# Kernel optimization log

Hardware: AMD Instinct MI355X
Metric: run time of the kernel (lower is better)

## Reference

```python
import jax, jax.numpy as jnp
import numpy as np

# Per-species MLP dims from CoefficientLayer._create_model (H, C, N, O), aev_dim=384
DIMS = {"h": [384, 160, 128, 96, 1], "c": [384, 144, 112, 96, 1], "n": [384, 128, 112, 96, 1], "o": [384, 128, 112, 96, 1]}


def setup_inputs() -> dict:
    key = jax.random.key(0)
    B, A, D = 256, 256, 384
    ks = jax.random.split(key, 64)
    inp = {}
    inp["species"] = jax.random.randint(ks[0], (B, A), 0, 4)  # species index 0..3
    inp["aev"] = jax.random.normal(ks[1], (B, A, D), dtype=jnp.float32)
    inp["b0"] = jnp.array([0.1, 0.2, 0.3, 0.4], dtype=jnp.float32)  # shifter intercepts
    inp["b1"] = jnp.array([1.0, 1.1, 0.9, 1.2], dtype=jnp.float32)  # shifter slopes
    ki = 2
    for name, dims in DIMS.items():
        for l in range(4):
            fi, fo = dims[l], dims[l + 1]
            inp[f"{name}w{l}"] = jax.random.normal(ks[ki], (fi, fo), dtype=jnp.float32) / np.float32(np.sqrt(fi))
            ki += 1
            inp[f"{name}b{l}"] = jnp.zeros((fo,), dtype=jnp.float32)
    return inp


def _mlp(x, ws, bs):
    # Linear -> CELU(0.1) x3 -> Linear(->1), squeeze last dim
    for i in range(3):
        x = jax.nn.celu(x @ ws[i] + bs[i], alpha=0.1)
    return (x @ ws[3] + bs[3])[..., 0]


def reference(species, aev, b0, b1,
              hw0, hb0, hw1, hb1, hw2, hb2, hw3, hb3,
              cw0, cb0, cw1, cb1, cw2, cb2, cw3, cb3,
              nw0, nb0, nw1, nb1, nw2, nb2, nw3, nb3,
              ow0, ob0, ow1, ob1, ow2, ob2, ow3, ob3):
    nets = [
        ([hw0, hw1, hw2, hw3], [hb0, hb1, hb2, hb3]),
        ([cw0, cw1, cw2, cw3], [cb0, cb1, cb2, cb3]),
        ([nw0, nw1, nw2, nw3], [nb0, nb1, nb2, nb3]),
        ([ow0, ow1, ow2, ow3], [ob0, ob1, ob2, ob3]),
    ]
    # ANIModel hard routing: each atom's coefficient comes from its species' network;
    # atoms with species == -1 (padding) stay 0.
    coef = jnp.zeros(species.shape, dtype=aev.dtype)
    for i, (ws, bs) in enumerate(nets):  # fixed small loop over 4 species
        coef = jnp.where(species == i, _mlp(aev, ws, bs), coef)
    # Shifter: result[mask_i] = b0[i] + b1[i] * coef[mask_i]; padding stays 0
    idx = jnp.clip(species, 0)
    return jnp.where(species >= 0, b0[idx] + b1[idx] * coef, jnp.zeros((), dtype=aev.dtype))
```

## Files before the change

kernel.cpp:

```cpp
#include <hip/hip_runtime.h>

typedef _Float16 f16;
typedef _Float16 f16x8 __attribute__((ext_vector_type(8)));
typedef float f32x4 __attribute__((ext_vector_type(4)));
typedef unsigned short u16;
typedef unsigned int u32;

#define NATOMS 65536
#define CAP 17920

#define WS_LISTS_OFF 256
#define WS_W_OFF 524544
#define WS_W_ELEMS 350208
#define WS_ACT0_OFF (2u << 20)
#define WS_BIG (46u << 20)

#define BLK0 128
#define BLK12 64

#define ROWB 1536
#define TILEB (16 * ROWB)
#define FRAGS 24

struct ConvJob { const float* src; int K, N, KS, NT, CK, off; };

struct PrepParams {
  const int* species;
  int* counts;
  u16* lists;
  f16* wbase;
  ConvJob jobs[16];
};

struct GemmParams {
  const float* aev;
  const float* b0;
  const float* b1;
  const float* bias[4][4];
  const float* w3src[4];
  const f16* w[4][4];
  const int* counts;
  const u16* lists;
  f16* act0;
  float* out;
  int Nreal0[4];
  int Nreal1[4];
};

template <int N> struct AF { f16x8 v[N]; };

__global__ __launch_bounds__(256) void prep_kernel(PrepParams p) {
  int tid = threadIdx.x;
  if (blockIdx.x < 256) {
    __shared__ int wcnt[4][4];
    __shared__ int wbase[4][4];
    int i = blockIdx.x * 256 + tid;
    int s = p.species[i];
    int wave = tid >> 6, lane = tid & 63;
    unsigned long long m[4];
    #pragma unroll
    for (int t = 0; t < 4; t++) {
      m[t] = __ballot(s == t);
      if (lane == 0) wcnt[wave][t] = __popcll(m[t]);
    }
    __syncthreads();
    if (tid < 4) {
      int t = tid;
      int c0 = wcnt[0][t], c1 = wcnt[1][t], c2 = wcnt[2][t], c3 = wcnt[3][t];
      int base = atomicAdd(&p.counts[t], c0 + c1 + c2 + c3);
      wbase[0][t] = base;
      wbase[1][t] = base + c0;
      wbase[2][t] = base + c0 + c1;
      wbase[3][t] = base + c0 + c1 + c2;
    }
    __syncthreads();
    int rnk = __popcll(m[s] & ((1ull << lane) - 1ull));
    p.lists[s * NATOMS + wbase[wave][s] + rnk] = (u16)i;
  } else {
    int bx = blockIdx.x - 256;
    int job = bx / 30, bxin = bx - job * 30;
    ConvJob jb = p.jobs[job];
    int e = bxin * 256 + tid;
    int nslots = jb.KS * jb.NT * 64;
    if (e >= nslots) return;
    int frag = e >> 6, lane = e & 63;
    int c = frag / (jb.CK * jb.NT);
    int rem = frag - c * (jb.CK * jb.NT);
    int ckc = min(jb.CK, jb.KS - c * jb.CK);
    int nt = rem / ckc, ki = rem - nt * ckc;
    int ks = c * jb.CK + ki;
    int q = lane >> 4, nlo = lane & 15;
    int n = nt * 16 + nlo;
    int k0 = ks * 32 + q * 8;
    f16x8 v;
    #pragma unroll
    for (int j = 0; j < 8; j++) {
      int k = k0 + j;
      float x = (n < jb.N && k < jb.K) ? jb.src[k * jb.N + n] : 0.f;
      v[j] = (f16)x;
    }
    *(f16x8*)(p.wbase + jb.off + (size_t)e * 8) = v;
  }
}

__device__ __forceinline__ float celu01(float v) {
  return v > 0.f ? v : 0.1f * (__expf(v * 10.f) - 1.f);
}

__device__ __forceinline__ void stage_frag(const f16* g, f16* l, int lane) {
  __builtin_amdgcn_global_load_lds(
      (const __attribute__((address_space(1))) u32*)(g + lane * 8),
      (__attribute__((address_space(3))) u32*)l, 16, 0, 0);
}

__device__ __forceinline__ void dma16(const void* g, void* l) {
  __builtin_amdgcn_global_load_lds(
      (const __attribute__((address_space(1))) u32*)g,
      (__attribute__((address_space(3))) u32*)l, 16, 0, 0);
}

template <int NT0>
__device__ void k0_body(const GemmParams& p, int s, int bl, char* smem) {
  int tid = threadIdx.x, w = tid >> 6, lane = tid & 63;
  int q = lane >> 4, nlo = lane & 15;
  int cnt = min(p.counts[s], CAP);
  int ntiles = (cnt + 15) >> 4;
  int tpb = (ntiles + BLK0 - 1) / BLK0;
  int t0 = bl * tpb;
  int nt_blk = min(ntiles - t0, tpb);
  if (nt_blk <= 0) return;

  const u16* list = p.lists + s * NATOMS;
  u16* atoms_l = (u16*)(smem + 3 * TILEB);

  f16x8 wf[12];
  float bv = 0.f;
  if (w < NT0) {
    const f16* wg = p.w[s][0];
    #pragma unroll
    for (int ks = 0; ks < 12; ks++)
      wf[ks] = *(const f16x8*)(wg + (size_t)(ks * NT0 + w) * 512 + lane * 8);
    int n = w * 16 + nlo;
    bv = (n < p.Nreal0[s]) ? p.bias[s][0][n] : 0.f;
  }
  f16* act = p.act0 + (size_t)s * CAP * 160;

  for (int idx = tid; idx < nt_blk * 16; idx += 640)
    atoms_l[idx] = list[min(t0 * 16 + idx, cnt - 1)];
  __syncthreads();

  auto stage = [&](int i) {
    char* buf = smem + (i % 3) * TILEB;
    #pragma unroll
    for (int j = 0; j < 3; j++) {
      int f = min(w * 3 + j, FRAGS - 1);
      int o = f * 1024 + lane * 16;
      int row = o / ROWB;
      int intra = o - row * ROWB;
      int gin = intra ^ ((row & 7) << 4);
      int atom = atoms_l[i * 16 + row];
      dma16((const char*)p.aev + (size_t)atom * ROWB + gin, buf + f * 1024);
    }
  };

  stage(0);
  if (nt_blk > 1) stage(1);
  for (int i = 0; i < nt_blk; i++) {
    if (i + 2 < nt_blk) {
      stage(i + 2);
      __builtin_amdgcn_s_waitcnt(0x0F73);
    } else {
      __builtin_amdgcn_s_waitcnt(0x0F70);
    }
    __builtin_amdgcn_s_barrier();
    asm volatile("" ::: "memory");
    if (w < NT0) {
      const char* buf = smem + (i % 3) * TILEB;
      int tb = (t0 + i) * 16;
      f32x4 acc = {0.f, 0.f, 0.f, 0.f};
      int base = nlo * ROWB + q * 32;
      int swz = (nlo & 7) << 4;
      #pragma unroll
      for (int ks = 0; ks < 12; ks++) {
        int lin = base + ks * 128;
        f32x4 u0 = *(const f32x4*)(buf + (lin ^ swz));
        f32x4 u1 = *(const f32x4*)(buf + ((lin + 16) ^ swz));
        f16x8 a = {(f16)u0[0], (f16)u0[1], (f16)u0[2], (f16)u0[3],
                   (f16)u1[0], (f16)u1[1], (f16)u1[2], (f16)u1[3]};
        acc = __builtin_amdgcn_mfma_f32_16x16x32_f16(a, wf[ks], acc, 0, 0, 0);
      }
      #pragma unroll
      for (int r = 0; r < 4; r++) {
        int row = tb + q * 4 + r;
        if (row < cnt)
          act[(size_t)row * 160 + w * 16 + nlo] = (f16)celu01(acc[r] + bv);
      }
    }
    asm volatile("" ::: "memory");
    __builtin_amdgcn_s_barrier();
  }
}

__global__ __launch_bounds__(640, 4) void k0_kernel(GemmParams p) {
  __shared__ __align__(16) char smem[3 * TILEB + 384];
  int s = blockIdx.x & 3, bl = blockIdx.x >> 2;
  switch (s) {
    case 0: k0_body<10>(p, 0, bl, smem); break;
    case 1: k0_body<10>(p, 1, bl, smem); break;
    case 2: k0_body<8>(p, 2, bl, smem); break;
    default: k0_body<8>(p, 3, bl, smem); break;
  }
}

template <int KS1>
__device__ void k12_body(const GemmParams& p, int s, int bl, f16* W1, f16* W2,
                         f16* T) {
  int tid = threadIdx.x, w = tid >> 6, lane = tid & 63;
  int q = lane >> 4, nlo = lane & 15;
  constexpr int NF1 = KS1 * 8;
  const f16* g1 = p.w[s][1];
  const f16* g2 = p.w[s][2];
  for (int f = w; f < NF1 + 24; f += 8) {
    if (f < NF1) stage_frag(g1 + (size_t)f * 512, W1 + f * 512, lane);
    else stage_frag(g2 + (size_t)(f - NF1) * 512, W2 + (f - NF1) * 512, lane);
  }
  int cnt = min(p.counts[s], CAP);
  int ntiles = (cnt + 15) >> 4;
  const u16* list = p.lists + s * NATOMS;
  int Nr1 = p.Nreal1[s];
  const float* bias1 = p.bias[s][1];
  const float* bias2 = p.bias[s][2];
  const float* w3 = p.w3src[s];
  float bv[8], b2v[6], w3v[6];
  #pragma unroll
  for (int nt = 0; nt < 8; nt++) {
    int n = nt * 16 + nlo;
    bv[nt] = (n < Nr1) ? bias1[n] : 0.f;
  }
  #pragma unroll
  for (int nt = 0; nt < 6; nt++) {
    int n = nt * 16 + nlo;
    b2v[nt] = bias2[n];
    w3v[nt] = w3[n];
  }
  float b3 = p.bias[s][3][0];
  float b0v = p.b0[s], b1v = p.b1[s];
  const f16* act0 = p.act0 + (size_t)s * CAP * 160;
  f16* Tw = T + (w * 16) * 160;
  __syncthreads();

  for (int t = bl * 8 + w; t < ntiles; t += BLK12 * 8) {
    int tb = t * 16;
    int ar = min(tb + nlo, cnt - 1);
    const f16* ap = act0 + (size_t)ar * 160 + q * 8;
    AF<KS1> a1;
    #pragma unroll
    for (int ks = 0; ks < KS1; ks++)
      a1.v[ks] = *(const f16x8*)(ap + ks * 32);
    f32x4 acc1[8];
    #pragma unroll
    for (int nt = 0; nt < 8; nt++) acc1[nt] = f32x4{0.f, 0.f, 0.f, 0.f};
    #pragma unroll
    for (int ks = 0; ks < KS1; ks++) {
      #pragma unroll
      for (int nt = 0; nt < 8; nt++) {
        f16x8 b = *(const f16x8*)(W1 + (ks * 8 + nt) * 512 + lane * 8);
        acc1[nt] = __builtin_amdgcn_mfma_f32_16x16x32_f16(a1.v[ks], b, acc1[nt], 0, 0, 0);
      }
    }
    #pragma unroll
    for (int nt = 0; nt < 8; nt++) {
      #pragma unroll
      for (int r = 0; r < 4; r++)
        Tw[(q * 4 + r) * 160 + nt * 16 + nlo] = (f16)celu01(acc1[nt][r] + bv[nt]);
    }
    AF<4> a2;
    #pragma unroll
    for (int ks = 0; ks < 4; ks++)
      a2.v[ks] = *(const f16x8*)(Tw + nlo * 160 + ks * 32 + q * 8);
    f32x4 acc2[6];
    #pragma unroll
    for (int nt = 0; nt < 6; nt++) acc2[nt] = f32x4{0.f, 0.f, 0.f, 0.f};
    #pragma unroll
    for (int ks = 0; ks < 4; ks++) {
      #pragma unroll
      for (int nt = 0; nt < 6; nt++) {
        f16x8 b = *(const f16x8*)(W2 + (ks * 6 + nt) * 512 + lane * 8);
        acc2[nt] = __builtin_amdgcn_mfma_f32_16x16x32_f16(a2.v[ks], b, acc2[nt], 0, 0, 0);
      }
    }
    float pr[4] = {0.f, 0.f, 0.f, 0.f};
    #pragma unroll
    for (int nt = 0; nt < 6; nt++) {
      #pragma unroll
      for (int r = 0; r < 4; r++) {
        float v = celu01(acc2[nt][r] + b2v[nt]);
        pr[r] += v * w3v[nt];
      }
    }
    #pragma unroll
    for (int m = 1; m < 16; m <<= 1) {
      #pragma unroll
      for (int r = 0; r < 4; r++) pr[r] += __shfl_xor(pr[r], m);
    }
    if (nlo == 0) {
      #pragma unroll
      for (int r = 0; r < 4; r++) {
        int row = tb + q * 4 + r;
        if (row < cnt) p.out[list[row]] = b0v + b1v * (pr[r] + b3);
      }
    }
  }
}

__global__ __launch_bounds__(512, 2) void k12_kernel(GemmParams p) {
  __shared__ __align__(16) f16 W1[5 * 8 * 512];
  __shared__ __align__(16) f16 W2[4 * 6 * 512];
  __shared__ __align__(16) f16 T[8 * 16 * 160];
  int s = blockIdx.x & 3, bl = blockIdx.x >> 2;
  switch (s) {
    case 0: k12_body<5>(p, 0, bl, W1, W2, T); break;
    case 1: k12_body<5>(p, 1, bl, W1, W2, T); break;
    case 2: k12_body<4>(p, 2, bl, W1, W2, T); break;
    default: k12_body<4>(p, 3, bl, W1, W2, T); break;
  }
}


extern "C" void kernel_launch(void* const* d_in, const int* in_sizes, int n_in,
                              void* d_out, int out_size, void* d_ws, size_t ws_size,
                              hipStream_t stream) {
  if (ws_size < WS_BIG) return;

  const int* species = (const int*)d_in[0];
  const float* aev = (const float*)d_in[1];
  const float* b0 = (const float*)d_in[2];
  const float* b1 = (const float*)d_in[3];

  static const int F1[4]  = {160, 144, 128, 128};
  static const int F1p[4] = {160, 160, 128, 128};
  static const int F2[4]  = {128, 112, 112, 112};

  char* wsb = (char*)d_ws;
  int* counts = (int*)wsb;
  u16* lists = (u16*)(wsb + WS_LISTS_OFF);
  f16* wbase = (f16*)(wsb + WS_W_OFF);

  PrepParams pp;
  pp.species = species; pp.counts = counts; pp.lists = lists; pp.wbase = wbase;

  GemmParams mp;
  mp.aev = aev; mp.b0 = b0; mp.b1 = b1;
  mp.counts = counts; mp.lists = lists; mp.out = (float*)d_out;
  mp.act0 = (f16*)(wsb + WS_ACT0_OFF);

  int off = 0, ji = 0;
  for (int s = 0; s < 4; s++) {
    int K[4]  = {384, F1[s], F2[s], 96};
    int N[4]  = {F1[s], F2[s], 96, 1};
    int KS[4] = {12, F1p[s] / 32, 4, 3};
    int NT[4] = {F1p[s] / 16, 8, 6, 1};
    int CK[4] = {1, 1, 1, 3};
    for (int l = 0; l < 4; l++) {
      const float* w = (const float*)d_in[4 + s * 8 + l * 2];
      const float* b = (const float*)d_in[4 + s * 8 + l * 2 + 1];
      pp.jobs[ji].src = w;
      pp.jobs[ji].K = K[l];
      pp.jobs[ji].N = N[l];
      pp.jobs[ji].KS = KS[l];
      pp.jobs[ji].NT = NT[l];
      pp.jobs[ji].CK = CK[l];
      pp.jobs[ji].off = off;
      mp.w[s][l] = wbase + off;
      mp.bias[s][l] = b;
      off += KS[l] * NT[l] * 512;
      ji++;
    }
    mp.w3src[s] = (const float*)d_in[4 + s * 8 + 6];
    mp.Nreal0[s] = F1[s];
    mp.Nreal1[s] = F2[s];
  }

  hipMemsetAsync(d_ws, 0, 64, stream);
  prep_kernel<<<dim3(256 + 480), 256, 0, stream>>>(pp);
  k0_kernel<<<dim3(4 * BLK0), 640, 0, stream>>>(mp);
  k12_kernel<<<dim3(4 * BLK12), 512, 0, stream>>>(mp);
}
```

Baseline: 262.2 us.

## Deepen k0 AEV prefetch, transpose MFMA output, prefetch next k12 activation tile

In k0, only the first 8 waves now issue the AEV gather DMA. The pipeline runs three tiles ahead, with the next stage issued after the trailing barrier and per-wave waitcnt values picked by remaining depth. The MFMA operands are swapped so each lane holds 4 consecutive output columns for one row, which lets the activation store become a single 8-byte vector write instead of four scattered 2-byte stores. In k12, the next tile's layer-1 activations are loaded before computing the current tile to hide global latency, at the cost of more registers.

```diff
diff --git a/kernel.cpp b/kernel.cpp
--- a/kernel.cpp
+++ b/kernel.cpp
@@ -1,6 +1,7 @@
 #include <hip/hip_runtime.h>
 
 typedef _Float16 f16;
+typedef _Float16 f16x4 __attribute__((ext_vector_type(4)));
 typedef _Float16 f16x8 __attribute__((ext_vector_type(8)));
 typedef float f32x4 __attribute__((ext_vector_type(4)));
 typedef unsigned short u16;
@@ -119,6 +120,17 @@
       (__attribute__((address_space(3))) u32*)l, 16, 0, 0);
 }
 
+__device__ __forceinline__ void wait_vm(int n) {
+  switch (n) {
+    case 0: __builtin_amdgcn_s_waitcnt(0x0F70); break;
+    case 1: __builtin_amdgcn_s_waitcnt(0x0F71); break;
+    case 3: __builtin_amdgcn_s_waitcnt(0x0F73); break;
+    case 4: __builtin_amdgcn_s_waitcnt(0x0F74); break;
+    case 6: __builtin_amdgcn_s_waitcnt(0x0F76); break;
+    default: __builtin_amdgcn_s_waitcnt(0x0F77); break;
+  }
+}
+
 template <int NT0>
 __device__ void k0_body(const GemmParams& p, int s, int bl, char* smem) {
   int tid = threadIdx.x, w = tid >> 6, lane = tid & 63;
@@ -134,14 +146,17 @@
   u16* atoms_l = (u16*)(smem + 3 * TILEB);
 
   f16x8 wf[12];
-  float bv = 0.f;
+  float bvv[4];
   if (w < NT0) {
     const f16* wg = p.w[s][0];
     #pragma unroll
     for (int ks = 0; ks < 12; ks++)
       wf[ks] = *(const f16x8*)(wg + (size_t)(ks * NT0 + w) * 512 + lane * 8);
-    int n = w * 16 + nlo;
-    bv = (n < p.Nreal0[s]) ? p.bias[s][0][n] : 0.f;
+    #pragma unroll
+    for (int r = 0; r < 4; r++) {
+      int n = w * 16 + q * 4 + r;
+      bvv[r] = (n < p.Nreal0[s]) ? p.bias[s][0][n] : 0.f;
+    }
   }
   f16* act = p.act0 + (size_t)s * CAP * 160;
 
@@ -153,7 +168,7 @@
     char* buf = smem + (i % 3) * TILEB;
     #pragma unroll
     for (int j = 0; j < 3; j++) {
-      int f = min(w * 3 + j, FRAGS - 1);
+      int f = w * 3 + j;
       int o = f * 1024 + lane * 16;
       int row = o / ROWB;
       int intra = o - row * ROWB;
@@ -163,14 +178,16 @@
     }
   };
 
-  stage(0);
-  if (nt_blk > 1) stage(1);
+  if (w < 8) {
+    stage(0);
+    if (nt_blk > 1) stage(1);
+    if (nt_blk > 2) stage(2);
+  }
+
   for (int i = 0; i < nt_blk; i++) {
-    if (i + 2 < nt_blk) {
-      stage(i + 2);
-      __builtin_amdgcn_s_waitcnt(0x0F73);
-    } else {
-      __builtin_amdgcn_s_waitcnt(0x0F70);
+    if (w < 8) {
+      int ahead = min(nt_blk - 1 - i, 2);
+      wait_vm(3 * ahead + (i > 0 ? 1 : 0));
     }
     __builtin_amdgcn_s_barrier();
     asm volatile("" ::: "memory");
@@ -187,17 +204,19 @@
         f32x4 u1 = *(const f32x4*)(buf + ((lin + 16) ^ swz));
         f16x8 a = {(f16)u0[0], (f16)u0[1], (f16)u0[2], (f16)u0[3],
                    (f16)u1[0], (f16)u1[1], (f16)u1[2], (f16)u1[3]};
-        acc = __builtin_amdgcn_mfma_f32_16x16x32_f16(a, wf[ks], acc, 0, 0, 0);
-      }
-      #pragma unroll
-      for (int r = 0; r < 4; r++) {
-        int row = tb + q * 4 + r;
-        if (row < cnt)
-          act[(size_t)row * 160 + w * 16 + nlo] = (f16)celu01(acc[r] + bv);
+        acc = __builtin_amdgcn_mfma_f32_16x16x32_f16(wf[ks], a, acc, 0, 0, 0);
+      }
+      int row = tb + nlo;
+      if (row < cnt) {
+        f16x4 o;
+        #pragma unroll
+        for (int r = 0; r < 4; r++) o[r] = (f16)celu01(acc[r] + bvv[r]);
+        *(f16x4*)(act + (size_t)row * 160 + w * 16 + q * 4) = o;
       }
     }
     asm volatile("" ::: "memory");
     __builtin_amdgcn_s_barrier();
+    if (w < 8 && i + 3 < nt_blk) stage(i + 3);
   }
 }
 
@@ -249,14 +268,24 @@
   f16* Tw = T + (w * 16) * 160;
   __syncthreads();
 
-  for (int t = bl * 8 + w; t < ntiles; t += BLK12 * 8) {
+  auto load_a1 = [&](int t) {
+    AF<KS1> a;
+    int ar = min(t * 16 + nlo, cnt - 1);
+    const f16* ap = act0 + (size_t)ar * 160 + q * 8;
+    #pragma unroll
+    for (int ks = 0; ks < KS1; ks++)
+      a.v[ks] = *(const f16x8*)(ap + ks * 32);
+    return a;
+  };
+
+  int t = bl * 8 + w;
+  if (t >= ntiles) return;
+  AF<KS1> a1 = load_a1(t);
+  while (true) {
+    int tn = t + BLK12 * 8;
+    AF<KS1> a1n;
+    if (tn < ntiles) a1n = load_a1(tn);
     int tb = t * 16;
-    int ar = min(tb + nlo, cnt - 1);
-    const f16* ap = act0 + (size_t)ar * 160 + q * 8;
-    AF<KS1> a1;
-    #pragma unroll
-    for (int ks = 0; ks < KS1; ks++)
-      a1.v[ks] = *(const f16x8*)(ap + ks * 32);
     f32x4 acc1[8];
     #pragma unroll
     for (int nt = 0; nt < 8; nt++) acc1[nt] = f32x4{0.f, 0.f, 0.f, 0.f};
@@ -310,6 +339,9 @@
         if (row < cnt) p.out[list[row]] = b0v + b1v * (pr[r] + b3);
       }
     }
+    if (tn >= ntiles) break;
+    a1 = a1n;
+    t = tn;
   }
 }
 
```

New measurement: 257.5 us. No clear change (-1.8%).
